# Kernel optimization log

Hardware: AMD Instinct MI355X
Metric: run time of the kernel (lower is better)

Reference implementation:

```python
import jax, jax.numpy as jnp
import numpy as np

B, S, D, H = 4, 2048, 1024, 16
DH = D // H  # 64


def setup_inputs() -> dict:
    key = jax.random.key(0)
    ks = jax.random.split(key, 9)
    hidden_states = jax.random.normal(ks[0], (B, S, D), dtype=jnp.float32)
    dis_mask = jax.random.randint(ks[1], (B, S, S), 0, 2, dtype=jnp.int32)
    # ensure no fully-masked row (diagonal visible)
    eye = jnp.eye(S, dtype=jnp.int32)[None]
    dis_mask = jnp.maximum(dis_mask, eye)
    relative_distance = jax.random.normal(ks[2], (B, S, S), dtype=jnp.float32)
    scale = 0.02
    Wq = jax.random.normal(ks[3], (D, D), dtype=jnp.float32) * scale
    bq = jnp.zeros((D,), dtype=jnp.float32)
    Wk = jax.random.normal(ks[4], (D, D), dtype=jnp.float32) * scale
    bk = jnp.zeros((D,), dtype=jnp.float32)
    Wv = jax.random.normal(ks[5], (D, D), dtype=jnp.float32) * scale
    bv = jnp.zeros((D,), dtype=jnp.float32)
    return {
        "hidden_states": hidden_states,
        "relative_distance": relative_distance,
        "Wq": Wq, "bq": bq, "Wk": Wk, "bk": bk, "Wv": Wv, "bv": bv,
        "dis_mask": dis_mask,
    }


def reference(hidden_states, relative_distance, Wq, bq, Wk, bk, Wv, bv, dis_mask):
    b, s, d = hidden_states.shape
    # nn.Linear: x @ W^T + b ; split heads -> [B,H,S,DH]
    def heads(x):
        return x.reshape(b, s, H, DH).transpose(0, 2, 1, 3)
    q = heads(hidden_states @ Wq.T + bq)
    k = heads(hidden_states @ Wk.T + bk)
    v = heads(hidden_states @ Wv.T + bv)
    scores = jnp.einsum('bhqd,bhkd->bhqk', q, k) / jnp.sqrt(jnp.float32(DH))
    # masked_fill(dis_mask == 0, -1e9) + relative_distance (pos=True path)
    masked = jnp.where(dis_mask[:, None, :, :] == 0, jnp.float32(-1e9), scores)
    masked = masked + relative_distance[:, None, :, :]
    probs = jax.nn.softmax(masked, axis=-1)  # dropout = identity (eval)
    ctx = jnp.einsum('bhqk,bhkd->bhqd', probs, v)
    ctx = ctx.transpose(0, 2, 1, 3).reshape(b, s, d)
    return ctx, jnp.mean(scores, axis=1)
```

## Files before the change

### kernel.cpp

```cpp
#include <hip/hip_runtime.h>
#include <hip/hip_bf16.h>
#include <stdint.h>


typedef __attribute__((ext_vector_type(4))) float f32x4;
typedef __attribute__((ext_vector_type(8))) short bf16x8;
typedef __attribute__((ext_vector_type(4))) unsigned int u32x4;

#define LOG2E 1.44269504088896f
constexpr int NS = 2048, ND = 1024, NDH = 64;

#define AS1U(p) (const __attribute__((address_space(1))) unsigned*)(p)
#define AS3U(p) (__attribute__((address_space(3))) unsigned*)(p)
#define GLD16(g, l) __builtin_amdgcn_global_load_lds(AS1U(g), AS3U(l), 16, 0, 0)

__device__ __forceinline__ unsigned short f2b(float f) {
  __hip_bfloat16 h = __float2bfloat16(f);
  return *reinterpret_cast<unsigned short*>(&h);
}

__global__ void cast_f32_bf16(const float* __restrict__ s, __hip_bfloat16* __restrict__ d, int n) {
  int i = (blockIdx.x * blockDim.x + threadIdx.x) * 4;
  if (i >= n) return;
  float4 v = *reinterpret_cast<const float4*>(s + i);
  ushort4 o;
  o.x = f2b(v.x); o.y = f2b(v.y); o.z = f2b(v.z); o.w = f2b(v.w);
  *reinterpret_cast<ushort4*>(d + i) = o;
}

__global__ void concat_bias(const float* __restrict__ bq, const float* __restrict__ bk,
                            const float* __restrict__ bv, float* __restrict__ dst) {
  int i = blockIdx.x * blockDim.x + threadIdx.x;
  const float* s = (i < 1024) ? bq : ((i < 2048) ? bk : bv);
  dst[i] = s[i & 1023];
}

__global__ void fuse_bias(const int* __restrict__ mk, float* __restrict__ rd, int n) {
  int i = (blockIdx.x * blockDim.x + threadIdx.x) * 4;
  if (i >= n) return;
  int4 m = *reinterpret_cast<const int4*>(mk + i);
  float4 r = *reinterpret_cast<const float4*>(rd + i);
  r.x = m.x ? r.x : -1e9f;
  r.y = m.y ? r.y : -1e9f;
  r.z = m.z ? r.z : -1e9f;
  r.w = m.w ? r.w : -1e9f;
  *reinterpret_cast<float4*>(rd + i) = r;
}

__global__ __launch_bounds__(256) void transpose_v(const __hip_bfloat16* __restrict__ V,
                                                   __hip_bfloat16* __restrict__ Vt) {
  __shared__ unsigned short T[64][64];
  const int st = blockIdx.x, h = blockIdx.y, b = blockIdx.z;
  const int t = threadIdx.x;
#pragma unroll
  for (int i = 0; i < 2; ++i) {
    int idx = i * 256 + t;
    int r = idx >> 3, cg = (idx & 7) * 8;
    bf16x8 v = *reinterpret_cast<const bf16x8*>(
        V + ((size_t)(b * 2048 + st * 64 + r)) * 1024 + h * 64 + cg);
    *reinterpret_cast<bf16x8*>(&T[r][cg ^ (((r >> 3) & 7) << 3)]) = v;
  }
  __syncthreads();
#pragma unroll
  for (int i = 0; i < 2; ++i) {
    int idx = i * 256 + t;
    int d = idx >> 3, sg = (idx & 7) * 8;
    bf16x8 o;
#pragma unroll
    for (int j = 0; j < 8; ++j) {
      int r = sg + j;
      o[j] = (short)T[r][d ^ (((r >> 3) & 7) << 3)];
    }
    *reinterpret_cast<bf16x8*>(Vt + ((size_t)((b * 16 + h) * 64 + d)) * 2048 + st * 64 + sg) = o;
  }
}

template <int EPI>
__global__ __launch_bounds__(256) void gemm_bt(
    const __hip_bfloat16* __restrict__ Ag, const __hip_bfloat16* __restrict__ Bg,
    const float* __restrict__ biasv, void* __restrict__ Cout, int Kdim, float scale) {
  __shared__ char Asm[128 * 128];
  __shared__ char Bsm[128 * 128];
  const int t = threadIdx.x;
  const int lane = t & 63, wid = t >> 6;
  const int fr = lane & 15, fg = lane >> 4;
  const int wr = wid >> 1, wc = wid & 1;
  const int m0 = blockIdx.x * 128, n0 = blockIdx.y * 128;
  const char* Ab = (const char*)Ag;
  const char* Bb = (const char*)Bg;
  if (EPI == 1) {
    size_t zoff = (size_t)blockIdx.z * NS * ND * 2;
    Ab += zoff; Bb += zoff;
  }
  const size_t rowbytes = (size_t)Kdim * 2;
  f32x4 acc[4][4] = {};
  for (int k0 = 0; k0 < Kdim; k0 += 64) {
    __syncthreads();
#pragma unroll
    for (int c = 0; c < 4; ++c) {
      int idx = c * 256 + t;
      int row = idx >> 3;
      int bc = (idx & 7) * 16;
      int sb = bc ^ ((row & 7) << 4);
      u32x4 va = *reinterpret_cast<const u32x4*>(Ab + (size_t)(m0 + row) * rowbytes + k0 * 2 + bc);
      *reinterpret_cast<u32x4*>(Asm + row * 128 + sb) = va;
      u32x4 vb = *reinterpret_cast<const u32x4*>(Bb + (size_t)(n0 + row) * rowbytes + k0 * 2 + bc);
      *reinterpret_cast<u32x4*>(Bsm + row * 128 + sb) = vb;
    }
    __syncthreads();
#pragma unroll
    for (int kk = 0; kk < 2; ++kk) {
      bf16x8 af[4], bfr[4];
      const int kb = (kk * 32 + fg * 8) * 2;
#pragma unroll
      for (int i = 0; i < 4; ++i) {
        int ar = wr * 64 + i * 16 + fr;
        af[i] = *reinterpret_cast<const bf16x8*>(Asm + ar * 128 + (kb ^ ((ar & 7) << 4)));
        int br = wc * 64 + i * 16 + fr;
        bfr[i] = *reinterpret_cast<const bf16x8*>(Bsm + br * 128 + (kb ^ ((br & 7) << 4)));
      }
#pragma unroll
      for (int i = 0; i < 4; ++i)
#pragma unroll
        for (int j = 0; j < 4; ++j)
          acc[i][j] = __builtin_amdgcn_mfma_f32_16x16x32_bf16(af[i], bfr[j], acc[i][j], 0, 0, 0);
    }
  }
  if (EPI == 0) {
    __hip_bfloat16* out = (__hip_bfloat16*)Cout;
#pragma unroll
    for (int i = 0; i < 4; ++i)
#pragma unroll
      for (int j = 0; j < 4; ++j) {
        int col = n0 + wc * 64 + j * 16 + fr;
        float bias = biasv[col];
        size_t obase = (size_t)(col >> 10) * 8388608 + (size_t)(col & 1023);
#pragma unroll
        for (int r = 0; r < 4; ++r) {
          int row = m0 + wr * 64 + i * 16 + fg * 4 + r;
          out[obase + (size_t)row * 1024] = __float2bfloat16(acc[i][j][r] + bias);
        }
      }
  } else {
    float* out = (float*)Cout + (size_t)blockIdx.z * NS * NS;
#pragma unroll
    for (int i = 0; i < 4; ++i)
#pragma unroll
      for (int j = 0; j < 4; ++j) {
        int col = n0 + wc * 64 + j * 16 + fr;
#pragma unroll
        for (int r = 0; r < 4; ++r) {
          int row = m0 + wr * 64 + i * 16 + fg * 4 + r;
          out[(size_t)row * NS + col] = acc[i][j][r] * scale;
        }
      }
  }
}

__global__ __launch_bounds__(256, 2) void attn3_kernel(
    const __hip_bfloat16* __restrict__ Qb, const __hip_bfloat16* __restrict__ Kb,
    const __hip_bfloat16* __restrict__ Vtg, const float* __restrict__ biasg,
    float* __restrict__ outc) {
  __shared__ char Ksm[2][8192];
  __shared__ char Vsm[2][8192];
  __shared__ char Bsm2[4][8192];
  __shared__ char Pl[4][4096];
  const int t = threadIdx.x;
  const int lane = t & 63, wid = t >> 6;
  const int fr = lane & 15, fg = lane >> 4;
  const int flat = blockIdx.x + (blockIdx.y << 4) + (blockIdx.z << 8);
  const int w = (flat & 7) * 128 + (flat >> 3);
  const int h = w & 15, qt = (w >> 4) & 15, b = w >> 8;
  const int q0 = qt * 128 + wid * 32;
  char* pbase = Pl[wid];
  char* bbase = Bsm2[wid];

  const __hip_bfloat16* Qp = Qb + (size_t)b * NS * ND + h * NDH;
  const __hip_bfloat16* Kp = Kb + (size_t)b * NS * ND + h * NDH;
  const __hip_bfloat16* Vt = Vtg + (size_t)(b * 16 + h) * 64 * NS;
  const float* Bp = biasg + ((size_t)b * NS + q0) * NS;

  int koff[2], voff[2], kldsb[2];
#pragma unroll
  for (int i = 0; i < 2; ++i) {
    int o = (i * 256 + t) * 8;
    int row = o >> 6, colS = o & 63;
    int col = colS ^ ((row & 7) << 3);
    koff[i] = row * ND + col;
    voff[i] = row * NS + col;
    kldsb[i] = o * 2;
  }
  int boff[8];
#pragma unroll
  for (int i = 0; i < 8; ++i) {
    int o = (i * 64 + lane) * 4;
    boff[i] = (o >> 6) * NS + (o & 63);
  }

  auto stageKV = [&](int k0n, int nb) {
#pragma unroll
    for (int i = 0; i < 2; ++i) {
      GLD16(Kp + (size_t)k0n * ND + koff[i], Ksm[nb] + kldsb[i]);
      GLD16(Vt + k0n + voff[i], Vsm[nb] + kldsb[i]);
    }
  };
  auto stageB = [&](int k0n) {
#pragma unroll
    for (int i = 0; i < 8; ++i)
      GLD16(Bp + boff[i] + k0n, bbase + (i * 64 + lane) * 16);
  };

  bf16x8 qf[2][2];
#pragma unroll
  for (int mi = 0; mi < 2; ++mi)
#pragma unroll
    for (int ki = 0; ki < 2; ++ki)
      qf[mi][ki] = *reinterpret_cast<const bf16x8*>(Qp + (size_t)(q0 + mi * 16 + fr) * ND + ki * 32 + fg * 8);

  f32x4 acc[2][4] = {};
  float mrun[2][4], lrun[2][4];
#pragma unroll
  for (int mi = 0; mi < 2; ++mi)
#pragma unroll
    for (int r = 0; r < 4; ++r) { mrun[mi][r] = -1e30f; lrun[mi][r] = 0.f; }

  stageKV(0, 0);
  stageB(0);
  int cur = 0;

  for (int kt = 0; kt < 32; ++kt) {
    const int k0 = kt * 64;
    __syncthreads();
    if (kt < 31) stageKV(k0 + 64, cur ^ 1);

    f32x4 sc[2][4] = {};
#pragma unroll
    for (int ki = 0; ki < 2; ++ki) {
      bf16x8 kf[4];
      const int kb = (ki * 32 + fg * 8) * 2;
#pragma unroll
      for (int ni = 0; ni < 4; ++ni) {
        int row = ni * 16 + fr;
        kf[ni] = *reinterpret_cast<const bf16x8*>(Ksm[cur] + row * 128 + (kb ^ ((row & 7) << 4)));
      }
#pragma unroll
      for (int mi = 0; mi < 2; ++mi)
#pragma unroll
        for (int ni = 0; ni < 4; ++ni)
          sc[mi][ni] = __builtin_amdgcn_mfma_f32_16x16x32_bf16(qf[mi][ki], kf[ni], sc[mi][ni], 0, 0, 0);
    }

#pragma unroll
    for (int mi = 0; mi < 2; ++mi)
#pragma unroll
      for (int r = 0; r < 4; ++r) {
        const char* brow = bbase + (mi * 16 + fg * 4 + r) * 256;
#pragma unroll
        for (int ni = 0; ni < 4; ++ni) {
          float bv = *reinterpret_cast<const float*>(brow + (ni * 16 + fr) * 4);
          sc[mi][ni][r] = sc[mi][ni][r] * 0.125f + bv;
        }
      }

#pragma unroll
    for (int mi = 0; mi < 2; ++mi)
#pragma unroll
      for (int r = 0; r < 4; ++r) {
        float v = fmaxf(fmaxf(sc[mi][0][r], sc[mi][1][r]), fmaxf(sc[mi][2][r], sc[mi][3][r]));
#pragma unroll
        for (int off = 8; off >= 1; off >>= 1) v = fmaxf(v, __shfl_xor(v, off, 16));
        float mold = mrun[mi][r];
        float mnew = fmaxf(mold, v);
        mrun[mi][r] = mnew;
        float scl = __builtin_exp2f((mold - mnew) * LOG2E);
        float rs = 0.f;
#pragma unroll
        for (int ni = 0; ni < 4; ++ni) {
          float p = __builtin_exp2f((sc[mi][ni][r] - mnew) * LOG2E);
          sc[mi][ni][r] = p;
          rs += p;
        }
#pragma unroll
        for (int off = 8; off >= 1; off >>= 1) rs += __shfl_xor(rs, off, 16);
        lrun[mi][r] = lrun[mi][r] * scl + rs;
#pragma unroll
        for (int di = 0; di < 4; ++di) acc[mi][di][r] *= scl;
      }

    __builtin_amdgcn_sched_barrier(0);
    if (kt < 31) stageB(k0 + 64);

#pragma unroll
    for (int mi = 0; mi < 2; ++mi)
#pragma unroll
      for (int ni = 0; ni < 4; ++ni)
#pragma unroll
        for (int r = 0; r < 4; ++r) {
          int prow = mi * 16 + fg * 4 + r;
          int pb = prow * 128 + (((ni * 16 + fr) * 2) ^ ((prow & 7) << 4));
          *reinterpret_cast<__hip_bfloat16*>(pbase + pb) = __float2bfloat16(sc[mi][ni][r]);
        }

#pragma unroll
    for (int kj = 0; kj < 2; ++kj) {
      bf16x8 pa[2], vf[4];
#pragma unroll
      for (int mi = 0; mi < 2; ++mi) {
        int pr2 = mi * 16 + fr;
        pa[mi] = *reinterpret_cast<const bf16x8*>(
            pbase + pr2 * 128 + (((kj * 32 + fg * 8) * 2) ^ ((pr2 & 7) << 4)));
      }
#pragma unroll
      for (int di = 0; di < 4; ++di) {
        int vr = di * 16 + fr;
        vf[di] = *reinterpret_cast<const bf16x8*>(
            Vsm[cur] + vr * 128 + (((kj * 32 + fg * 8) * 2) ^ ((vr & 7) << 4)));
      }
#pragma unroll
      for (int mi = 0; mi < 2; ++mi)
#pragma unroll
        for (int di = 0; di < 4; ++di)
          acc[mi][di] = __builtin_amdgcn_mfma_f32_16x16x32_bf16(pa[mi], vf[di], acc[mi][di], 0, 0, 0);
    }
    cur ^= 1;
  }

#pragma unroll
  for (int mi = 0; mi < 2; ++mi) {
    float rinv[4];
#pragma unroll
    for (int r = 0; r < 4; ++r) rinv[r] = 1.0f / lrun[mi][r];
#pragma unroll
    for (int di = 0; di < 4; ++di)
#pragma unroll
      for (int r = 0; r < 4; ++r) {
        size_t o = ((size_t)b * NS + q0 + mi * 16 + fg * 4 + r) * ND + h * NDH + di * 16 + fr;
        outc[o] = acc[mi][di][r] * rinv[r];
      }
  }
}

extern "C" void kernel_launch(void* const* d_in, const int* in_sizes, int n_in,
                              void* d_out, int out_size, void* d_ws, size_t ws_size,
                              hipStream_t stream) {
  (void)in_sizes; (void)n_in; (void)out_size; (void)ws_size;
  const float* hidden = (const float*)d_in[0];
  float*       rdist  = (float*)d_in[1];
  const float* Wq = (const float*)d_in[2];
  const float* bq = (const float*)d_in[3];
  const float* Wk = (const float*)d_in[4];
  const float* bk = (const float*)d_in[5];
  const float* Wv = (const float*)d_in[6];
  const float* bv = (const float*)d_in[7];
  const int* mask = (const int*)d_in[8];
  float* out = (float*)d_out;

  char* ws = (char*)d_ws;
  __hip_bfloat16* Xbf = (__hip_bfloat16*)(ws);
  __hip_bfloat16* Wbf = (__hip_bfloat16*)(ws + 16777216);
  float*          bcat = (float*)(ws + 23068672);
  __hip_bfloat16* Qbf = (__hip_bfloat16*)(ws + 23085056);
  __hip_bfloat16* Kbf = (__hip_bfloat16*)(ws + 23085056 + 16777216);
  __hip_bfloat16* Vbf = (__hip_bfloat16*)(ws + 23085056 + 33554432);
  __hip_bfloat16* Vt = Xbf;

  cast_f32_bf16<<<8192, 256, 0, stream>>>(hidden, Xbf, 8388608);
  cast_f32_bf16<<<1024, 256, 0, stream>>>(Wq, Wbf, 1048576);
  cast_f32_bf16<<<1024, 256, 0, stream>>>(Wk, Wbf + 1048576, 1048576);
  cast_f32_bf16<<<1024, 256, 0, stream>>>(Wv, Wbf + 2097152, 1048576);
  concat_bias<<<3, 1024, 0, stream>>>(bq, bk, bv, bcat);
  gemm_bt<0><<<dim3(64, 24, 1), 256, 0, stream>>>(Xbf, Wbf, bcat, (void*)Qbf, 1024, 0.f);
  transpose_v<<<dim3(32, 16, 4), 256, 0, stream>>>(Vbf, Vt);
  gemm_bt<1><<<dim3(16, 16, 4), 256, 0, stream>>>(Qbf, Kbf, nullptr,
                                                  (void*)(out + 8388608), 1024, 1.0f / 128.0f);
  fuse_bias<<<16384, 256, 0, stream>>>(mask, rdist, 16777216);
  attn3_kernel<<<dim3(16, 16, 4), 256, 0, stream>>>(Qbf, Kbf, Vt, rdist, out);
}
```

Measured before the change: 643.4 us.

## Permute fused bias layout so attention reads it directly into registers

The mask+bias fusion kernel now writes each 64-column chunk in a permuted order, so every lane's four bias values for its MFMA fragment are contiguous. The attention kernel then loads the bias straight from global memory as float4s per row, dropping the per-wave LDS bias staging buffers. Freeing that 32KB of LDS lets the launch bound go from 2 to 3 blocks per CU. The trade-off is that bias loads are now issued synchronously inside the loop rather than prefetched asynchronously, and the permuted fuse kernel does scalar scattered stores instead of one float4 store.

```diff
diff --git a/kernel.cpp b/kernel.cpp
--- a/kernel.cpp
+++ b/kernel.cpp
@@ -35,16 +35,21 @@
   dst[i] = s[i & 1023];
 }
 
-__global__ void fuse_bias(const int* __restrict__ mk, float* __restrict__ rd, int n) {
+__global__ void fuse_bias_perm(const int* __restrict__ mk, float* __restrict__ rd, int n) {
   int i = (blockIdx.x * blockDim.x + threadIdx.x) * 4;
   if (i >= n) return;
   int4 m = *reinterpret_cast<const int4*>(mk + i);
   float4 r = *reinterpret_cast<const float4*>(rd + i);
-  r.x = m.x ? r.x : -1e9f;
-  r.y = m.y ? r.y : -1e9f;
-  r.z = m.z ? r.z : -1e9f;
-  r.w = m.w ? r.w : -1e9f;
-  *reinterpret_cast<float4*>(rd + i) = r;
+  float v0 = m.x ? r.x : -1e9f;
+  float v1 = m.y ? r.y : -1e9f;
+  float v2 = m.z ? r.z : -1e9f;
+  float v3 = m.w ? r.w : -1e9f;
+  int base = i & ~63;
+  int cw = i & 63;
+  rd[base + ((cw + 0) & 15) * 4 + ((cw + 0) >> 4)] = v0;
+  rd[base + ((cw + 1) & 15) * 4 + ((cw + 1) >> 4)] = v1;
+  rd[base + ((cw + 2) & 15) * 4 + ((cw + 2) >> 4)] = v2;
+  rd[base + ((cw + 3) & 15) * 4 + ((cw + 3) >> 4)] = v3;
 }
 
 __global__ __launch_bounds__(256) void transpose_v(const __hip_bfloat16* __restrict__ V,
@@ -157,13 +162,12 @@
   }
 }
 
-__global__ __launch_bounds__(256, 2) void attn3_kernel(
+__global__ __launch_bounds__(256, 3) void attn4_kernel(
     const __hip_bfloat16* __restrict__ Qb, const __hip_bfloat16* __restrict__ Kb,
     const __hip_bfloat16* __restrict__ Vtg, const float* __restrict__ biasg,
     float* __restrict__ outc) {
   __shared__ char Ksm[2][8192];
   __shared__ char Vsm[2][8192];
-  __shared__ char Bsm2[4][8192];
   __shared__ char Pl[4][4096];
   const int t = threadIdx.x;
   const int lane = t & 63, wid = t >> 6;
@@ -173,7 +177,6 @@
   const int h = w & 15, qt = (w >> 4) & 15, b = w >> 8;
   const int q0 = qt * 128 + wid * 32;
   char* pbase = Pl[wid];
-  char* bbase = Bsm2[wid];
 
   const __hip_bfloat16* Qp = Qb + (size_t)b * NS * ND + h * NDH;
   const __hip_bfloat16* Kp = Kb + (size_t)b * NS * ND + h * NDH;
@@ -190,12 +193,6 @@
     voff[i] = row * NS + col;
     kldsb[i] = o * 2;
   }
-  int boff[8];
-#pragma unroll
-  for (int i = 0; i < 8; ++i) {
-    int o = (i * 64 + lane) * 4;
-    boff[i] = (o >> 6) * NS + (o & 63);
-  }
 
   auto stageKV = [&](int k0n, int nb) {
 #pragma unroll
@@ -204,11 +201,6 @@
       GLD16(Vt + k0n + voff[i], Vsm[nb] + kldsb[i]);
     }
   };
-  auto stageB = [&](int k0n) {
-#pragma unroll
-    for (int i = 0; i < 8; ++i)
-      GLD16(Bp + boff[i] + k0n, bbase + (i * 64 + lane) * 16);
-  };
 
   bf16x8 qf[2][2];
 #pragma unroll
@@ -225,7 +217,6 @@
     for (int r = 0; r < 4; ++r) { mrun[mi][r] = -1e30f; lrun[mi][r] = 0.f; }
 
   stageKV(0, 0);
-  stageB(0);
   int cur = 0;
 
   for (int kt = 0; kt < 32; ++kt) {
@@ -233,6 +224,14 @@
     __syncthreads();
     if (kt < 31) stageKV(k0 + 64, cur ^ 1);
 
+    f32x4 bfrag[2][4];
+#pragma unroll
+    for (int mi = 0; mi < 2; ++mi)
+#pragma unroll
+      for (int r = 0; r < 4; ++r)
+        bfrag[mi][r] = *reinterpret_cast<const f32x4*>(
+            Bp + (size_t)(mi * 16 + fg * 4 + r) * NS + k0 + fr * 4);
+
     f32x4 sc[2][4] = {};
 #pragma unroll
     for (int ki = 0; ki < 2; ++ki) {
@@ -253,14 +252,10 @@
 #pragma unroll
     for (int mi = 0; mi < 2; ++mi)
 #pragma unroll
-      for (int r = 0; r < 4; ++r) {
-        const char* brow = bbase + (mi * 16 + fg * 4 + r) * 256;
-#pragma unroll
-        for (int ni = 0; ni < 4; ++ni) {
-          float bv = *reinterpret_cast<const float*>(brow + (ni * 16 + fr) * 4);
-          sc[mi][ni][r] = sc[mi][ni][r] * 0.125f + bv;
-        }
-      }
+      for (int r = 0; r < 4; ++r)
+#pragma unroll
+        for (int ni = 0; ni < 4; ++ni)
+          sc[mi][ni][r] = sc[mi][ni][r] * 0.125f + bfrag[mi][r][ni];
 
 #pragma unroll
     for (int mi = 0; mi < 2; ++mi)
@@ -286,9 +281,6 @@
 #pragma unroll
         for (int di = 0; di < 4; ++di) acc[mi][di][r] *= scl;
       }
-
-    __builtin_amdgcn_sched_barrier(0);
-    if (kt < 31) stageB(k0 + 64);
 
 #pragma unroll
     for (int mi = 0; mi < 2; ++mi)
@@ -373,6 +365,6 @@
   transpose_v<<<dim3(32, 16, 4), 256, 0, stream>>>(Vbf, Vt);
   gemm_bt<1><<<dim3(16, 16, 4), 256, 0, stream>>>(Qbf, Kbf, nullptr,
                                                   (void*)(out + 8388608), 1024, 1.0f / 128.0f);
-  fuse_bias<<<16384, 256, 0, stream>>>(mask, rdist, 16777216);
-  attn3_kernel<<<dim3(16, 16, 4), 256, 0, stream>>>(Qbf, Kbf, Vt, rdist, out);
-}
+  fuse_bias_perm<<<16384, 256, 0, stream>>>(mask, rdist, 16777216);
+  attn4_kernel<<<dim3(16, 16, 4), 256, 0, stream>>>(Qbf, Kbf, Vt, rdist, out);
+}
```

Result: slower. 740.6 us (+15.1%).
